# Performance work log

Measured on AMD Instinct MI355X. Metric: run time of the kernel, lower is better.

The kernel has to match this reference:

```python
import jax, jax.numpy as jnp
import numpy as np
from jax import lax

B, L = 128, 256
DW, DC = 100, 30
H = 400          # hidden_size (bidirectional total)
HD = H // 2      # per-direction hidden
NT = 18          # tag vocab size (BIOES)
VW, VC = 400000, 50000


def setup_inputs():
    key = jax.random.key(0)
    ks = iter(jax.random.split(key, 64))
    rn = lambda shape, s=0.1: jax.random.normal(next(ks), shape, jnp.float32) * s
    inp = {
        "words": jax.random.randint(next(ks), (B, L), 0, VW),
        "cap_words": jax.random.randint(next(ks), (B, L), 0, VC),
        "seq_len": jax.random.randint(next(ks), (B,), L // 2, L + 1),
        "target": jax.random.randint(next(ks), (B, L), 0, NT),
        "word_emb": rn((VW, DW)),
        "char_emb": rn((VC, DC)),
    }
    for l, din in ((0, DW + DC), (1, H)):
        for d in ("f", "b"):
            inp[f"W_ih_l{l}{d}"] = rn((4 * HD, din))
            inp[f"W_hh_l{l}{d}"] = rn((4 * HD, HD))
            inp[f"b_ih_l{l}{d}"] = rn((4 * HD,))
            inp[f"b_hh_l{l}{d}"] = rn((4 * HD,))
    inp["Wf"], inp["bf"] = rn((NT, HD)), jnp.zeros((NT,), jnp.float32)
    inp["Wb"], inp["bb"] = rn((NT, HD)), jnp.zeros((NT,), jnp.float32)
    inp["trans"] = rn((NT, NT))
    return inp


def _lstm_dir(x, W_ih, W_hh, b_ih, b_hh):
    # x: [B, L, D] -> hidden states [B, L, HD]; torch gate order i, f, g, o
    Bsz = x.shape[0]
    def step(carry, xt):
        h, c = carry
        g = xt @ W_ih.T + b_ih + h @ W_hh.T + b_hh
        i, f, gg, o = jnp.split(g, 4, axis=-1)
        c = jax.nn.sigmoid(f) * c + jax.nn.sigmoid(i) * jnp.tanh(gg)
        h = jax.nn.sigmoid(o) * jnp.tanh(c)
        return (h, c), h
    init = (jnp.zeros((Bsz, HD), x.dtype), jnp.zeros((Bsz, HD), x.dtype))
    _, hs = lax.scan(step, init, jnp.swapaxes(x, 0, 1))
    return jnp.swapaxes(hs, 0, 1)


def _rev(x, seq_len):
    # reverse each sequence within its true length (padding stays in place),
    # emulating pack_padded_sequence semantics for the backward direction
    t = jnp.arange(x.shape[1])[None, :]
    idx = jnp.where(t < seq_len[:, None], seq_len[:, None] - 1 - t, t)
    return jnp.take_along_axis(x, idx[:, :, None], axis=1)


def _crf_nll(logits, tags, mask, trans):
    # normalizer: forward algorithm, logsumexp scan over time with mask
    def step(alpha, inp):
        emit, m = inp  # emit: [B, NT], m: [B] bool
        new = jax.nn.logsumexp(alpha[:, :, None] + trans[None] + emit[:, None, :], axis=1)
        return jnp.where(m[:, None], new, alpha), None
    emits = jnp.swapaxes(logits, 0, 1)  # [L, B, NT]
    ms = jnp.swapaxes(mask, 0, 1)
    alpha, _ = lax.scan(step, emits[0], (emits[1:], ms[1:]))
    z = jax.nn.logsumexp(alpha, axis=1)
    # gold path score
    mf = mask.astype(logits.dtype)
    emit_sc = jnp.take_along_axis(logits, tags[:, :, None], axis=2)[:, :, 0]
    gold = jnp.sum(emit_sc * mf, axis=1) + jnp.sum(trans[tags[:, :-1], tags[:, 1:]] * mf[:, 1:], axis=1)
    return z - gold  # per-sample negative log-likelihood, shape [B]


def _model(words, cap_words, seq_len, target, word_emb, char_emb,
           W_ih_l0f, W_hh_l0f, b_ih_l0f, b_hh_l0f, W_ih_l0b, W_hh_l0b, b_ih_l0b, b_hh_l0b,
           W_ih_l1f, W_hh_l1f, b_ih_l1f, b_hh_l1f, W_ih_l1b, W_hh_l1b, b_ih_l1b, b_hh_l1b,
           Wf, bf, Wb, bb, trans):
    mask = jnp.arange(L)[None, :] < seq_len[:, None]  # [B, L] bool
    mf = mask.astype(jnp.float32)[:, :, None]
    x = jnp.concatenate([word_emb[words], char_emb[cap_words]], axis=-1)
    layers = (((W_ih_l0f, W_hh_l0f, b_ih_l0f, b_hh_l0f), (W_ih_l0b, W_hh_l0b, b_ih_l0b, b_hh_l0b)),
              ((W_ih_l1f, W_hh_l1f, b_ih_l1f, b_hh_l1f), (W_ih_l1b, W_hh_l1b, b_ih_l1b, b_hh_l1b)))
    h = x
    for fp, bp in layers:
        fwd = _lstm_dir(h, *fp)
        bwd = _rev(_lstm_dir(_rev(h, seq_len), *bp), seq_len)
        h = jnp.concatenate([fwd, bwd], axis=-1) * mf  # zero padded steps like packed LSTM
    forwards, backwards = h[..., :HD], h[..., HD:]
    logits = forwards @ Wf.T + bf + backwards @ Wb.T + bb
    return _crf_nll(logits, target, mask, trans)


def reference(words, cap_words, seq_len, target, word_emb, char_emb,
              W_ih_l0f, W_hh_l0f, b_ih_l0f, b_hh_l0f, W_ih_l0b, W_hh_l0b, b_ih_l0b, b_hh_l0b,
              W_ih_l1f, W_hh_l1f, b_ih_l1f, b_hh_l1f, W_ih_l1b, W_hh_l1b, b_ih_l1b, b_hh_l1b,
              Wf, bf, Wb, bb, trans):
    return _model(words, cap_words, seq_len, target, word_emb, char_emb,
                  W_ih_l0f, W_hh_l0f, b_ih_l0f, b_hh_l0f, W_ih_l0b, W_hh_l0b, b_ih_l0b, b_hh_l0b,
                  W_ih_l1f, W_hh_l1f, b_ih_l1f, b_hh_l1f, W_ih_l1b, W_hh_l1b, b_ih_l1b, b_hh_l1b,
                  Wf, bf, Wb, bb, trans)
```

## Files before the change

### kernel.cpp

```cpp
#include <hip/hip_runtime.h>
#include <math.h>

#define B_   128
#define L_   256
#define DW_  100
#define DC_  30
#define HD_  200
#define NT_  18
#define SG   4
#define KP0  160
#define KP1  416

typedef _Float16 half8 __attribute__((ext_vector_type(8)));
typedef _Float16 half4 __attribute__((ext_vector_type(4)));
typedef float    f32x4 __attribute__((ext_vector_type(4)));

__device__ __forceinline__ float frcp_(float x) { return __builtin_amdgcn_rcpf(x); }
__device__ __forceinline__ float sigm_(float x) { return frcp_(1.0f + __expf(-x)); }
__device__ __forceinline__ float tanh_(float x) { return 1.0f - 2.0f * frcp_(1.0f + __expf(2.0f * x)); }

__device__ __forceinline__ void barrier_lgkm() {
    asm volatile("s_waitcnt lgkmcnt(0)" ::: "memory");
    __builtin_amdgcn_s_barrier();
    asm volatile("" ::: "memory");
}

__global__ __launch_bounds__(128) void k_sortperm(const int* __restrict__ seq_len,
                                                  int* __restrict__ perm) {
    __shared__ int s[B_];
    int i = threadIdx.x;
    s[i] = seq_len[i];
    __syncthreads();
    int key = s[i], r = 0;
    for (int j = 0; j < B_; j++) {
        int v = s[j];
        r += (v < key) || (v == key && j < i);
    }
    perm[r] = i;
}

__global__ void k_embed(const int* __restrict__ words, const int* __restrict__ caps,
                        const float* __restrict__ wemb, const float* __restrict__ cemb,
                        _Float16* __restrict__ x) {
    int pos = blockIdx.x;
    int w = words[pos], c = caps[pos];
    _Float16* xp = x + (size_t)pos * KP0;
    for (int t = threadIdx.x; t < KP0; t += blockDim.x) {
        float v = 0.f;
        if (t < DW_) v = wemb[(size_t)w * DW_ + t];
        else if (t < DW_ + DC_) v = cemb[(size_t)c * DC_ + (t - DW_)];
        xp[t] = (_Float16)v;
    }
}

__global__ void k_perm_ih16(const float* __restrict__ src, _Float16* __restrict__ dst,
                            int K, int Kpad, int colOff) {
    int i = blockIdx.x * blockDim.x + threadIdx.x;
    if (i >= 800 * Kpad) return;
    int r = i / Kpad, k = i - r * Kpad;
    int jh = r % 200, g = r / 200;
    int col = colOff + (jh << 2) + g;
    dst[(size_t)col * Kpad + k] = (k < K) ? (_Float16)src[(size_t)r * K + k] : (_Float16)0.f;
}

__global__ void k_bias_perm(const float* bi_f, const float* bh_f,
                            const float* bi_b, const float* bh_b, float* bias) {
    int j = blockIdx.x * blockDim.x + threadIdx.x;
    if (j >= 1600) return;
    int dir = j / 800, r = j - dir * 800;
    int col = dir * 800 + ((r % 200) << 2) + (r / 200);
    bias[col] = dir ? (bi_b[r] + bh_b[r]) : (bi_f[r] + bh_f[r]);
}

__global__ void k_wlog(const float* __restrict__ Wf, const float* __restrict__ bfv,
                       const float* __restrict__ Wb, const float* __restrict__ bbv,
                       float* __restrict__ wlog, float* __restrict__ blog) {
    int i = blockIdx.x * blockDim.x + threadIdx.x;
    if (i < NT_ * 400) {
        int t = i / 400, k = i - t * 400;
        wlog[i] = (k < HD_) ? Wf[t * HD_ + k] : Wb[t * HD_ + (k - HD_)];
    }
    if (i < NT_) blog[i] = bfv[i] + bbv[i];
}

__global__ __launch_bounds__(256) void k_gemm16(const _Float16* __restrict__ A,
                                                const _Float16* __restrict__ Bt,
                                                const float* __restrict__ bias,
                                                _Float16* __restrict__ C,
                                                int Kpad) {
    __shared__ __align__(16) _Float16 sA[128 * 40];
    __shared__ __align__(16) _Float16 sB[64 * 40];
    const int tid = threadIdx.x;
    const int w = tid >> 6, l = tid & 63, l15 = l & 15, lq = l >> 4;
    const int m0 = blockIdx.y * 128, n0 = blockIdx.x * 64;
    const int rw = (w >> 1) * 64, cw = (w & 1) * 32;
    f32x4 acc[4][2];
    #pragma unroll
    for (int i = 0; i < 4; i++)
        #pragma unroll
        for (int j = 0; j < 2; j++) acc[i][j] = f32x4{0.f, 0.f, 0.f, 0.f};

    for (int k0 = 0; k0 < Kpad; k0 += 32) {
        {
            int m = tid >> 1, c = (tid & 1) << 4;
            const _Float16* ap = A + (size_t)(m0 + m) * Kpad + k0 + c;
            *(half8*)&sA[m * 40 + c]     = *(const half8*)ap;
            *(half8*)&sA[m * 40 + c + 8] = *(const half8*)(ap + 8);
        }
        {
            int n = tid >> 2, k8 = (tid & 3) << 3;
            *(half8*)&sB[n * 40 + k8] = *(const half8*)&Bt[(size_t)(n0 + n) * Kpad + k0 + k8];
        }
        __syncthreads();
        half8 aF[4], bF[2];
        #pragma unroll
        for (int i = 0; i < 4; i++) aF[i] = *(const half8*)&sA[(rw + i * 16 + l15) * 40 + lq * 8];
        #pragma unroll
        for (int j = 0; j < 2; j++) bF[j] = *(const half8*)&sB[(cw + j * 16 + l15) * 40 + lq * 8];
        #pragma unroll
        for (int i = 0; i < 4; i++)
            #pragma unroll
            for (int j = 0; j < 2; j++)
                acc[i][j] = __builtin_amdgcn_mfma_f32_16x16x32_f16(aF[i], bF[j], acc[i][j], 0, 0, 0);
        __syncthreads();
    }
    #pragma unroll
    for (int j = 0; j < 2; j++) {
        int n = n0 + cw + j * 16 + l15;
        float bv = bias[n];
        #pragma unroll
        for (int i = 0; i < 4; i++) {
            int mrow = m0 + rw + i * 16 + lq * 4;
            #pragma unroll
            for (int r = 0; r < 4; r++)
                C[(size_t)(mrow + r) * 1600 + n] = (_Float16)(acc[i][j][r] + bv);
        }
    }
}

__global__ __launch_bounds__(512) void k_scan10(const _Float16* __restrict__ gates,
                                                const float* __restrict__ Whh_f,
                                                const float* __restrict__ Whh_b,
                                                const int* __restrict__ seq_len,
                                                const int* __restrict__ perm,
                                                _Float16* __restrict__ hout, int ldH) {
    const int dir = blockIdx.x & 1;
    const int b0  = (blockIdx.x >> 1) * SG;
    const int tid = threadIdx.x;
    const int w   = tid >> 6;
    const int l   = tid & 63;
    const int l15 = l & 15;
    const int lq  = l >> 4;

    __shared__ __align__(16) _Float16 hA[2][16 * 232];
    __shared__ __align__(16) _Float16 bEx[2 * 7 * 512];
    __shared__ __align__(16) float    gD[8 * 448];
    __shared__ int ssl[SG];
    __shared__ int spb[SG];

    const float* W = dir ? Whh_b : Whh_f;
    const int nT = (w < 2) ? 7 : 6;
    const int nCell = nT * 16;

    half8 Breg[6][7];
    #pragma unroll
    for (int i = 0; i < 6; i++) {
        int n  = (w * 6 + i) * 16 + l15;
        int jh = n >> 2, g = n & 3;
        const float* Wr = W + (size_t)(g * 200 + jh) * 200;
        #pragma unroll
        for (int kt = 0; kt < 7; kt++) {
            int k0 = kt * 32 + lq * 8;
            half8 f;
            #pragma unroll
            for (int j = 0; j < 8; j++) {
                int k = k0 + j;
                f[j] = (k < 200) ? (_Float16)Wr[k] : (_Float16)0.f;
            }
            Breg[i][kt] = f;
        }
    }
    if (w < 2) {
        int n  = (48 + w) * 16 + l15;
        int jh = n >> 2, g = n & 3;
        const float* Wr = W + (size_t)(g * 200 + jh) * 200;
        for (int kt = 0; kt < 7; kt++) {
            int k0 = kt * 32 + lq * 8;
            half8 f;
            for (int j = 0; j < 8; j++) {
                int k = k0 + j;
                f[j] = (k < 200) ? (_Float16)Wr[k] : (_Float16)0.f;
            }
            *(half8*)&bEx[(w * 7 + kt) * 512 + l * 8] = f;
        }
    }
    for (int i = tid; i < 2 * 16 * 232; i += 512) (&hA[0][0])[i] = (_Float16)0.f;
    if (tid < SG) {
        int ob = perm[b0 + tid];
        spb[tid] = ob;
        ssl[tid] = seq_len[ob];
    }

    const int  v    = tid;
    const bool stv  = v < 400;
    const int  m_st = v / 100;
    const int  u_st = v - m_st * 100;

    const int cA = l;
    const int iA = cA >> 4, qA = (cA >> 2) & 3, mA = cA & 3;
    const int tgA = (iA < 6) ? (w * 6 + iA) : (48 + w);
    const int hcA = tgA * 4 + qA;
    const int cB = l + 64;
    const int iB = cB >> 4, qB = (cB >> 2) & 3, mB = cB & 3;
    const bool vB = cB < nCell;
    const int tgB = (iB < 6) ? (w * 6 + iB) : (48 + w);
    const int hcB = tgB * 4 + qB;
    float csA = 0.f, csB = 0.f;

    __syncthreads();

    const int slmax = max(max(ssl[0], ssl[1]), max(ssl[2], ssl[3]));

    const int slA = ssl[mA];
    const int slB = ssl[mB];
    const int slb_st = stv ? ssl[m_st] : 0;
    const _Float16* gA_base = gates + ((size_t)spb[mA] * L_) * 1600 + dir * 800 + 4 * hcA;
    const _Float16* gB_base = gates + ((size_t)spb[mB] * L_) * 1600 + dir * 800 + 4 * hcB;
    _Float16* hout_base = stv ? (hout + (size_t)spb[m_st] * L_ * ldH + dir * HD_ + 2 * u_st)
                              : hout;

    auto rowOf = [&](int t, int sl) -> int {
        return dir ? ((t < sl) ? sl - 1 - t : t) : t;
    };

    half4 gA0, gA1, gB0, gB1;
    gA0 = *(const half4*)(gA_base + (size_t)rowOf(0, slA) * 1600);
    gA1 = *(const half4*)(gA_base + (size_t)rowOf(1, slA) * 1600);
    if (vB) {
        gB0 = *(const half4*)(gB_base + (size_t)rowOf(0, slB) * 1600);
        gB1 = *(const half4*)(gB_base + (size_t)rowOf(1, slB) * 1600);
    }

    const f32x4 Cz = {0.f, 0.f, 0.f, 0.f};
    for (int t = 0; t < slmax; t++) {
        const int p = t & 1;

        if (t > 0 && stv) {
            int tp = t - 1;
            int row = dir ? ((tp < slb_st) ? slb_st - 1 - tp : tp) : tp;
            unsigned int val = (tp < slb_st) ? *(const unsigned int*)&hA[p][m_st * 232 + 2 * u_st] : 0u;
            *(unsigned int*)(hout_base + (size_t)row * ldH) = val;
        }

        f32x4 C[7];
        #pragma unroll
        for (int i = 0; i < 7; i++) C[i] = Cz;
        #pragma unroll
        for (int kt = 0; kt < 7; kt++) {
            half8 hF = *(const half8*)&hA[p][l15 * 232 + kt * 32 + lq * 8];
            #pragma unroll
            for (int i = 0; i < 6; i++)
                C[i] = __builtin_amdgcn_mfma_f32_16x16x32_f16(Breg[i][kt], hF, C[i], 0, 0, 0);
            if (w < 2) {
                half8 bF = *(const half8*)&bEx[(w * 7 + kt) * 512 + l * 8];
                C[6] = __builtin_amdgcn_mfma_f32_16x16x32_f16(bF, hF, C[6], 0, 0, 0);
            }
        }

        if (l15 < 4) {
            #pragma unroll
            for (int i = 0; i < 6; i++)
                *(f32x4*)&gD[w * 448 + (i * 16 + lq * 4 + l15) * 4] = C[i];
            if (w < 2)
                *(f32x4*)&gD[w * 448 + (6 * 16 + lq * 4 + l15) * 4] = C[6];
        }

        {
            f32x4 gv = *(const f32x4*)&gD[w * 448 + cA * 4];
            float xi = gv[0] + (float)gA0[0];
            float xf = gv[1] + (float)gA0[1];
            float xg = gv[2] + (float)gA0[2];
            float xo = gv[3] + (float)gA0[3];
            float cn = sigm_(xf) * csA + sigm_(xi) * tanh_(xg);
            csA = cn;
            hA[1 - p][mA * 232 + hcA] = (_Float16)(sigm_(xo) * tanh_(cn));
        }
        if (vB) {
            f32x4 gv = *(const f32x4*)&gD[w * 448 + cB * 4];
            float xi = gv[0] + (float)gB0[0];
            float xf = gv[1] + (float)gB0[1];
            float xg = gv[2] + (float)gB0[2];
            float xo = gv[3] + (float)gB0[3];
            float cn = sigm_(xf) * csB + sigm_(xi) * tanh_(xg);
            csB = cn;
            hA[1 - p][mB * 232 + hcB] = (_Float16)(sigm_(xo) * tanh_(cn));
        }

        gA0 = gA1;
        gB0 = gB1;
        if (t + 2 < L_) {
            gA1 = *(const half4*)(gA_base + (size_t)rowOf(t + 2, slA) * 1600);
            if (vB) gB1 = *(const half4*)(gB_base + (size_t)rowOf(t + 2, slB) * 1600);
        }

        barrier_lgkm();
    }
    if (stv) {
        int tp = slmax - 1;
        int row = dir ? ((tp < slb_st) ? slb_st - 1 - tp : tp) : tp;
        unsigned int val = (tp < slb_st) ? *(const unsigned int*)&hA[slmax & 1][m_st * 232 + 2 * u_st] : 0u;
        *(unsigned int*)(hout_base + (size_t)row * ldH) = val;
    }
    if (stv) {
        for (int tp = slmax; tp < L_; tp++)
            *(unsigned int*)(hout_base + (size_t)tp * ldH) = 0u;
    }
}

__global__ __launch_bounds__(256) void k_logits(const _Float16* __restrict__ h1,
                                                const float* __restrict__ wlog,
                                                const float* __restrict__ blog,
                                                float* __restrict__ logits) {
    __shared__ float sh[8][400];
    __shared__ float sw[NT_ * 400];
    int p0 = blockIdx.x * 8;
    for (int i = threadIdx.x; i < 8 * 400; i += 256)
        sh[i / 400][i % 400] = (float)h1[(size_t)p0 * 400 + i];
    for (int i = threadIdx.x; i < NT_ * 400; i += 256) sw[i] = wlog[i];
    __syncthreads();
    if (threadIdx.x < 8 * NT_) {
        int pi = threadIdx.x / NT_, tg = threadIdx.x % NT_;
        float a = blog[tg];
        #pragma unroll 4
        for (int k = 0; k < 400; k++) a += sh[pi][k] * sw[tg * 400 + k];
        logits[((size_t)(p0 + pi)) * NT_ + tg] = a;
    }
}

__global__ __launch_bounds__(64) void k_crf(const float* __restrict__ logits,
                                            const int* __restrict__ target,
                                            const int* __restrict__ seq_len,
                                            const float* __restrict__ trans,
                                            float* __restrict__ out) {
    int b = blockIdx.x, tid = threadIdx.x;
    __shared__ float alpha[NT_];
    int sl = seq_len[b];
    const float* lg = logits + (size_t)b * L_ * NT_;
    const int* tg = target + (size_t)b * L_;

    const bool act = tid < 54;
    const int c = tid / 18, j = tid - c * 18;

    float Tl[6];
    #pragma unroll
    for (int k = 0; k < 6; k++)
        Tl[k] = act ? trans[(6 * c + k) * NT_ + j] : 0.f;

    float gacc = 0.f;
    for (int t = tid; t < L_; t += 64) {
        if (t < sl) {
            gacc += lg[t * NT_ + tg[t]];
            if (t >= 1) gacc += trans[tg[t - 1] * NT_ + tg[t]];
        }
    }
    #pragma unroll
    for (int off = 32; off; off >>= 1) gacc += __shfl_down(gacc, off);
    float gold = __shfl(gacc, 0);

    if (tid < NT_) alpha[tid] = lg[tid];

    const int src1 = (c < 2) ? tid + 18 : tid - 36;
    const int src2 = (c == 0) ? tid + 36 : tid - 18;

    for (int t = 1; t < sl; t++) {
        float m = -1e30f, s = 0.f;
        if (act) {
            float v0 = alpha[6 * c + 0] + Tl[0];
            float v1 = alpha[6 * c + 1] + Tl[1];
            float v2 = alpha[6 * c + 2] + Tl[2];
            float v3 = alpha[6 * c + 3] + Tl[3];
            float v4 = alpha[6 * c + 4] + Tl[4];
            float v5 = alpha[6 * c + 5] + Tl[5];
            m = fmaxf(fmaxf(fmaxf(v0, v1), fmaxf(v2, v3)), fmaxf(v4, v5));
            s = __expf(v0 - m) + __expf(v1 - m) + __expf(v2 - m) +
                __expf(v3 - m) + __expf(v4 - m) + __expf(v5 - m);
        }
        float m1 = __shfl(m, src1), s1 = __shfl(s, src1);
        float m2 = __shfl(m, src2), s2 = __shfl(s, src2);
        if (act && c == 0) {
            float M = fmaxf(m, fmaxf(m1, m2));
            float S = s * __expf(m - M) + s1 * __expf(m1 - M) + s2 * __expf(m2 - M);
            alpha[j] = M + __logf(S) + lg[t * NT_ + j];
        }
    }
    if (tid == 0) {
        float mx = -1e30f;
        for (int i = 0; i < NT_; i++) mx = fmaxf(mx, alpha[i]);
        float s = 0.f;
        for (int i = 0; i < NT_; i++) s += __expf(alpha[i] - mx);
        out[b] = (mx + __logf(s)) - gold;
    }
}

extern "C" void kernel_launch(void* const* d_in, const int* in_sizes, int n_in,
                              void* d_out, int out_size, void* d_ws, size_t ws_size,
                              hipStream_t stream) {
    const int*   words  = (const int*)d_in[0];
    const int*   caps   = (const int*)d_in[1];
    const int*   seq    = (const int*)d_in[2];
    const int*   target = (const int*)d_in[3];
    const float* wemb   = (const float*)d_in[4];
    const float* cemb   = (const float*)d_in[5];
    const float* Wih0f  = (const float*)d_in[6];
    const float* Whh0f  = (const float*)d_in[7];
    const float* bih0f  = (const float*)d_in[8];
    const float* bhh0f  = (const float*)d_in[9];
    const float* Wih0b  = (const float*)d_in[10];
    const float* Whh0b  = (const float*)d_in[11];
    const float* bih0b  = (const float*)d_in[12];
    const float* bhh0b  = (const float*)d_in[13];
    const float* Wih1f  = (const float*)d_in[14];
    const float* Whh1f  = (const float*)d_in[15];
    const float* bih1f  = (const float*)d_in[16];
    const float* bhh1f  = (const float*)d_in[17];
    const float* Wih1b  = (const float*)d_in[18];
    const float* Whh1b  = (const float*)d_in[19];
    const float* bih1b  = (const float*)d_in[20];
    const float* bhh1b  = (const float*)d_in[21];
    const float* Wf     = (const float*)d_in[22];
    const float* bfv    = (const float*)d_in[23];
    const float* Wb     = (const float*)d_in[24];
    const float* bbv    = (const float*)d_in[25];
    const float* trans  = (const float*)d_in[26];

    char* base = (char*)d_ws;
    _Float16* gatesH = (_Float16*)(base + 0);
    _Float16* xbuf   = (_Float16*)(base + 104857600);
    _Float16* h0b    = (_Float16*)(base + 115343360);
    _Float16* h1b    = xbuf;
    float* logitsb   = (float*)(base + 142606336);
    _Float16* wihT0  = (_Float16*)(base + 144965632);
    _Float16* wihT1  = (_Float16*)(base + 145477632);
    float* bias0     = (float*)(base + 146808832);
    float* bias1     = (float*)(base + 146815232);
    float* wlog      = (float*)(base + 146821632);
    float* blog      = (float*)(base + 146850432);
    int*   permb     = (int*)(base + 146850560);

    k_perm_ih16<<<(800 * KP0 + 255) / 256, 256, 0, stream>>>(Wih0f, wihT0, 130, KP0, 0);
    k_perm_ih16<<<(800 * KP0 + 255) / 256, 256, 0, stream>>>(Wih0b, wihT0, 130, KP0, 800);
    k_perm_ih16<<<(800 * KP1 + 255) / 256, 256, 0, stream>>>(Wih1f, wihT1, 400, KP1, 0);
    k_perm_ih16<<<(800 * KP1 + 255) / 256, 256, 0, stream>>>(Wih1b, wihT1, 400, KP1, 800);
    k_bias_perm<<<7, 256, 0, stream>>>(bih0f, bhh0f, bih0b, bhh0b, bias0);
    k_bias_perm<<<7, 256, 0, stream>>>(bih1f, bhh1f, bih1b, bhh1b, bias1);
    k_wlog<<<(NT_ * 400 + 255) / 256, 256, 0, stream>>>(Wf, bfv, Wb, bbv, wlog, blog);
    k_sortperm<<<1, 128, 0, stream>>>(seq, permb);

    k_embed<<<B_ * L_, 128, 0, stream>>>(words, caps, wemb, cemb, xbuf);

    hipMemsetAsync(h0b, 0, (size_t)32768 * KP1 * sizeof(_Float16), stream);

    k_gemm16<<<dim3(25, 256), 256, 0, stream>>>(xbuf, wihT0, bias0, gatesH, KP0);
    k_scan10<<<(B_ / SG) * 2, 512, 0, stream>>>(gatesH, Whh0f, Whh0b, seq, permb, h0b, KP1);

    k_gemm16<<<dim3(25, 256), 256, 0, stream>>>(h0b, wihT1, bias1, gatesH, KP1);
    k_scan10<<<(B_ / SG) * 2, 512, 0, stream>>>(gatesH, Whh1f, Whh1b, seq, permb, h1b, 400);

    k_logits<<<(B_ * L_) / 8, 256, 0, stream>>>(h1b, wlog, blog, logitsb);
    k_crf<<<B_, 64, 0, stream>>>(logitsb, target, seq, trans, (float*)d_out);
}
```

Baseline: 1.422 ms.

## Pack 16 sequences per LSTM scan block and apply gates directly from MFMA accumulators

The recurrent scan kernel now handles 16 batch sequences per block instead of 4, so every column of the 16-wide MFMA tile holds a real sequence. The grid shrinks from 64 to 16 blocks. The LDS staging buffer that redistributed gate pre-activations is removed, and each lane applies the LSTM cell update straight from its accumulator registers, loading its input-gate values per step rather than prefetching them two steps ahead. The intent is to cut MFMA work wasted on padding and the extra LDS round trip, at the cost of fewer blocks, less GPU parallelism, and every block running to the longest of 16 sequences.

```diff
diff --git a/kernel.cpp b/kernel.cpp
--- a/kernel.cpp
+++ b/kernel.cpp
@@ -7,7 +7,7 @@
 #define DC_  30
 #define HD_  200
 #define NT_  18
-#define SG   4
+#define SG   16
 #define KP0  160
 #define KP1  416
 
@@ -138,7 +138,7 @@
     }
 }
 
-__global__ __launch_bounds__(512) void k_scan10(const _Float16* __restrict__ gates,
+__global__ __launch_bounds__(512) void k_scan11(const _Float16* __restrict__ gates,
                                                 const float* __restrict__ Whh_f,
                                                 const float* __restrict__ Whh_b,
                                                 const int* __restrict__ seq_len,
@@ -154,13 +154,10 @@
 
     __shared__ __align__(16) _Float16 hA[2][16 * 232];
     __shared__ __align__(16) _Float16 bEx[2 * 7 * 512];
-    __shared__ __align__(16) float    gD[8 * 448];
     __shared__ int ssl[SG];
     __shared__ int spb[SG];
 
     const float* W = dir ? Whh_b : Whh_f;
-    const int nT = (w < 2) ? 7 : 6;
-    const int nCell = nT * 16;
 
     half8 Breg[6][7];
     #pragma unroll
@@ -201,55 +198,49 @@
         ssl[tid] = seq_len[ob];
     }
 
-    const int  v    = tid;
-    const bool stv  = v < 400;
-    const int  m_st = v / 100;
-    const int  u_st = v - m_st * 100;
-
-    const int cA = l;
-    const int iA = cA >> 4, qA = (cA >> 2) & 3, mA = cA & 3;
-    const int tgA = (iA < 6) ? (w * 6 + iA) : (48 + w);
-    const int hcA = tgA * 4 + qA;
-    const int cB = l + 64;
-    const int iB = cB >> 4, qB = (cB >> 2) & 3, mB = cB & 3;
-    const bool vB = cB < nCell;
-    const int tgB = (iB < 6) ? (w * 6 + iB) : (48 + w);
-    const int hcB = tgB * 4 + qB;
-    float csA = 0.f, csB = 0.f;
-
     __syncthreads();
 
-    const int slmax = max(max(ssl[0], ssl[1]), max(ssl[2], ssl[3]));
-
-    const int slA = ssl[mA];
-    const int slB = ssl[mB];
-    const int slb_st = stv ? ssl[m_st] : 0;
-    const _Float16* gA_base = gates + ((size_t)spb[mA] * L_) * 1600 + dir * 800 + 4 * hcA;
-    const _Float16* gB_base = gates + ((size_t)spb[mB] * L_) * 1600 + dir * 800 + 4 * hcB;
-    _Float16* hout_base = stv ? (hout + (size_t)spb[m_st] * L_ * ldH + dir * HD_ + 2 * u_st)
-                              : hout;
-
-    auto rowOf = [&](int t, int sl) -> int {
-        return dir ? ((t < sl) ? sl - 1 - t : t) : t;
-    };
-
-    half4 gA0, gA1, gB0, gB1;
-    gA0 = *(const half4*)(gA_base + (size_t)rowOf(0, slA) * 1600);
-    gA1 = *(const half4*)(gA_base + (size_t)rowOf(1, slA) * 1600);
-    if (vB) {
-        gB0 = *(const half4*)(gB_base + (size_t)rowOf(0, slB) * 1600);
-        gB1 = *(const half4*)(gB_base + (size_t)rowOf(1, slB) * 1600);
-    }
-
+    int slmax = 0;
+    #pragma unroll
+    for (int j = 0; j < SG; j++) slmax = max(slmax, ssl[j]);
+
+    const int sl_c = ssl[l15];
+    const _Float16* gbase = gates + (size_t)spb[l15] * L_ * 1600 + dir * 800 + 4 * lq;
+
+    const int m_st = tid >> 5;
+    const int u0   = tid & 31;
+    const int sl_st = ssl[m_st];
+    _Float16* hout_b = hout + (size_t)spb[m_st] * L_ * ldH + dir * HD_;
+
+    float cs[7] = {0.f, 0.f, 0.f, 0.f, 0.f, 0.f, 0.f};
     const f32x4 Cz = {0.f, 0.f, 0.f, 0.f};
+
     for (int t = 0; t < slmax; t++) {
         const int p = t & 1;
 
-        if (t > 0 && stv) {
+        half4 gc[7];
+        {
+            int grow = dir ? ((t < sl_c) ? sl_c - 1 - t : t) : t;
+            const _Float16* gR = gbase + (size_t)grow * 1600;
+            #pragma unroll
+            for (int i = 0; i < 6; i++)
+                gc[i] = *(const half4*)(gR + 16 * (w * 6 + i));
+            if (w < 2) gc[6] = *(const half4*)(gR + 16 * (48 + w));
+        }
+
+        if (t > 0) {
             int tp = t - 1;
-            int row = dir ? ((tp < slb_st) ? slb_st - 1 - tp : tp) : tp;
-            unsigned int val = (tp < slb_st) ? *(const unsigned int*)&hA[p][m_st * 232 + 2 * u_st] : 0u;
-            *(unsigned int*)(hout_base + (size_t)row * ldH) = val;
+            bool live = tp < sl_st;
+            int row = dir ? (live ? sl_st - 1 - tp : tp) : tp;
+            _Float16* ho = hout_b + (size_t)row * ldH;
+            #pragma unroll
+            for (int k = 0; k < 4; k++) {
+                int u = u0 + 32 * k;
+                if (u < 100) {
+                    unsigned int val = live ? *(const unsigned int*)&hA[p][m_st * 232 + 2 * u] : 0u;
+                    *(unsigned int*)(ho + 2 * u) = val;
+                }
+            }
         }
 
         f32x4 C[7];
@@ -267,53 +258,50 @@
             }
         }
 
-        if (l15 < 4) {
-            #pragma unroll
-            for (int i = 0; i < 6; i++)
-                *(f32x4*)&gD[w * 448 + (i * 16 + lq * 4 + l15) * 4] = C[i];
-            if (w < 2)
-                *(f32x4*)&gD[w * 448 + (6 * 16 + lq * 4 + l15) * 4] = C[6];
-        }
-
-        {
-            f32x4 gv = *(const f32x4*)&gD[w * 448 + cA * 4];
-            float xi = gv[0] + (float)gA0[0];
-            float xf = gv[1] + (float)gA0[1];
-            float xg = gv[2] + (float)gA0[2];
-            float xo = gv[3] + (float)gA0[3];
-            float cn = sigm_(xf) * csA + sigm_(xi) * tanh_(xg);
-            csA = cn;
-            hA[1 - p][mA * 232 + hcA] = (_Float16)(sigm_(xo) * tanh_(cn));
-        }
-        if (vB) {
-            f32x4 gv = *(const f32x4*)&gD[w * 448 + cB * 4];
-            float xi = gv[0] + (float)gB0[0];
-            float xf = gv[1] + (float)gB0[1];
-            float xg = gv[2] + (float)gB0[2];
-            float xo = gv[3] + (float)gB0[3];
-            float cn = sigm_(xf) * csB + sigm_(xi) * tanh_(xg);
-            csB = cn;
-            hA[1 - p][mB * 232 + hcB] = (_Float16)(sigm_(xo) * tanh_(cn));
-        }
-
-        gA0 = gA1;
-        gB0 = gB1;
-        if (t + 2 < L_) {
-            gA1 = *(const half4*)(gA_base + (size_t)rowOf(t + 2, slA) * 1600);
-            if (vB) gB1 = *(const half4*)(gB_base + (size_t)rowOf(t + 2, slB) * 1600);
+        #pragma unroll
+        for (int i = 0; i < 6; i++) {
+            float xi = C[i][0] + (float)gc[i][0];
+            float xf = C[i][1] + (float)gc[i][1];
+            float xg = C[i][2] + (float)gc[i][2];
+            float xo = C[i][3] + (float)gc[i][3];
+            float cn = sigm_(xf) * cs[i] + sigm_(xi) * tanh_(xg);
+            cs[i] = cn;
+            hA[1 - p][l15 * 232 + (w * 6 + i) * 4 + lq] = (_Float16)(sigm_(xo) * tanh_(cn));
+        }
+        if (w < 2) {
+            float xi = C[6][0] + (float)gc[6][0];
+            float xf = C[6][1] + (float)gc[6][1];
+            float xg = C[6][2] + (float)gc[6][2];
+            float xo = C[6][3] + (float)gc[6][3];
+            float cn = sigm_(xf) * cs[6] + sigm_(xi) * tanh_(xg);
+            cs[6] = cn;
+            hA[1 - p][l15 * 232 + (48 + w) * 4 + lq] = (_Float16)(sigm_(xo) * tanh_(cn));
         }
 
         barrier_lgkm();
     }
-    if (stv) {
+
+    {
         int tp = slmax - 1;
-        int row = dir ? ((tp < slb_st) ? slb_st - 1 - tp : tp) : tp;
-        unsigned int val = (tp < slb_st) ? *(const unsigned int*)&hA[slmax & 1][m_st * 232 + 2 * u_st] : 0u;
-        *(unsigned int*)(hout_base + (size_t)row * ldH) = val;
-    }
-    if (stv) {
-        for (int tp = slmax; tp < L_; tp++)
-            *(unsigned int*)(hout_base + (size_t)tp * ldH) = 0u;
+        bool live = tp < sl_st;
+        int row = dir ? (live ? sl_st - 1 - tp : tp) : tp;
+        _Float16* ho = hout_b + (size_t)row * ldH;
+        #pragma unroll
+        for (int k = 0; k < 4; k++) {
+            int u = u0 + 32 * k;
+            if (u < 100) {
+                unsigned int val = live ? *(const unsigned int*)&hA[slmax & 1][m_st * 232 + 2 * u] : 0u;
+                *(unsigned int*)(ho + 2 * u) = val;
+            }
+        }
+    }
+    for (int tp = slmax; tp < L_; tp++) {
+        _Float16* ho = hout_b + (size_t)tp * ldH;
+        #pragma unroll
+        for (int k = 0; k < 4; k++) {
+            int u = u0 + 32 * k;
+            if (u < 100) *(unsigned int*)(ho + 2 * u) = 0u;
+        }
     }
 }
 
@@ -461,10 +449,10 @@
     hipMemsetAsync(h0b, 0, (size_t)32768 * KP1 * sizeof(_Float16), stream);
 
     k_gemm16<<<dim3(25, 256), 256, 0, stream>>>(xbuf, wihT0, bias0, gatesH, KP0);
-    k_scan10<<<(B_ / SG) * 2, 512, 0, stream>>>(gatesH, Whh0f, Whh0b, seq, permb, h0b, KP1);
+    k_scan11<<<(B_ / SG) * 2, 512, 0, stream>>>(gatesH, Whh0f, Whh0b, seq, permb, h0b, KP1);
 
     k_gemm16<<<dim3(25, 256), 256, 0, stream>>>(h0b, wihT1, bias1, gatesH, KP1);
-    k_scan10<<<(B_ / SG) * 2, 512, 0, stream>>>(gatesH, Whh1f, Whh1b, seq, permb, h1b, 400);
+    k_scan11<<<(B_ / SG) * 2, 512, 0, stream>>>(gatesH, Whh1f, Whh1b, seq, permb, h1b, 400);
 
     k_logits<<<(B_ * L_) / 8, 256, 0, stream>>>(h1b, wlog, blog, logitsb);
     k_crf<<<B_, 64, 0, stream>>>(logitsb, target, seq, trans, (float*)d_out);
```

New measurement: 3.030 ms. 113% more time.
